# Kernel optimization log

Hardware: AMD Instinct MI355X
Metric: run time of the kernel (lower is better)

Reference implementation:

```python
import jax, jax.numpy as jnp
import numpy as np

EPS = 1e-5


def _conv1x1_3d(x, w, b):
    # x: [B,C,T,H,W], w: [O,C], b: [O]  (Conv3d with kernel 1)
    return jnp.einsum('bcthw,oc->bothw', x, w) + b[None, :, None, None, None]


def _nonlocal_layer(x, Kw, Kb, Qw, Qb, Vw, Vb, Ow, Ob, gamma, beta, in_dim):
    K = _conv1x1_3d(x, Kw, Kb)
    Q = _conv1x1_3d(x, Qw, Qb)
    V = _conv1x1_3d(x, Vw, Vb)
    B, C, T, H, W = K.shape
    S = T * H * W
    Kf = K.reshape(B, C, S)
    Qf = Q.reshape(B, C, S)
    Vf = V.reshape(B, C, S)
    # KQ[b,s,t] = sum_c K[b,c,s] Q[b,c,t];  attn = softmax over t
    attn = jax.nn.softmax(jnp.einsum('bcs,bct->bst', Kf, Qf) / np.sqrt(in_dim).astype(np.float32), axis=2)
    # original broadcast pattern: (V.view(B,C,S,1) * attn[:,None]).sum(3)
    #   == V[b,c,s] * sum_t attn[b,s,t]  (rows of softmax sum to ~1)
    Vn = Vf * attn.sum(axis=2)[:, None, :]
    Vn = jax.nn.relu(Vn).reshape(B, C, T, H, W)
    O = jax.nn.relu(_conv1x1_3d(Vn, Ow, Ob))
    y = x + O
    # BatchNorm3d in training mode: per-channel batch statistics
    mu = y.mean(axis=(0, 2, 3, 4), keepdims=True)
    var = y.var(axis=(0, 2, 3, 4), keepdims=True)
    return gamma[None, :, None, None, None] * (y - mu) / jnp.sqrt(var + EPS) + beta[None, :, None, None, None]


def _conv_transpose_2x2_s2(x, w, b):
    # torch ConvTranspose2d(k=2, stride=2): weight [Cin, Cout, 2, 2]; output pixels don't overlap
    N, C, H, W = x.shape
    O = w.shape[1]
    y = jnp.einsum('nchw,codk->nohdwk', x, w).reshape(N, O, 2 * H, 2 * W)
    return y + b[None, :, None, None]


def _positional_encoding(S, D):
    position = jnp.arange(S, dtype=jnp.float32)[:, None]
    div_term = jnp.exp(jnp.arange(0, D, 2, dtype=jnp.float32) * (-np.log(10000.0) / D))
    pe = jnp.zeros((S, D), dtype=jnp.float32)
    pe = pe.at[:, 0::2].set(jnp.sin(position * div_term))
    pe = pe.at[:, 1::2].set(jnp.cos(position * div_term))
    return pe  # [S, D]


def setup_inputs() -> dict:
    key = jax.random.key(0)
    ks = jax.random.split(key, 24)
    B, Tc, Hc, Wc = 8, 6, 12, 12
    Tf, Hf, Wf = 4, 12, 12
    Din, Dff, Dout, L = 1024, 512, 128, 2
    s = 0.02
    inp = {
        'context': jax.random.normal(ks[0], (B, Tc, Din, Hc, Wc), jnp.float32),
        'frame': jax.random.normal(ks[1], (B, Tf, Din, Hf, Wf), jnp.float32),
        'nl_Kw': jax.random.normal(ks[2], (L, Dff, Din), jnp.float32) * s,
        'nl_Kb': jnp.zeros((L, Dff), jnp.float32),
        'nl_Qw': jax.random.normal(ks[3], (L, Dff, Din), jnp.float32) * s,
        'nl_Qb': jnp.zeros((L, Dff), jnp.float32),
        'nl_Vw': jax.random.normal(ks[4], (L, Dff, Din), jnp.float32) * s,
        'nl_Vb': jnp.zeros((L, Dff), jnp.float32),
        'nl_Ow': jax.random.normal(ks[5], (L, Din, Dff), jnp.float32) * s,
        'nl_Ob': jnp.zeros((L, Din), jnp.float32),
        'nl_gamma': jnp.ones((L, Din), jnp.float32),
        'nl_beta': jnp.zeros((L, Din), jnp.float32),
        'tp_w': jax.random.normal(ks[6], (Dout, Din, 3, 3, 3), jnp.float32) * s,
        'tp_b': jnp.zeros((Dout,), jnp.float32),
        'up1_w': jax.random.normal(ks[7], (Din, Dff, 2, 2), jnp.float32) * s,
        'up1_b': jnp.zeros((Dff,), jnp.float32),
        'up2_w': jax.random.normal(ks[8], (Dff, Dout, 2, 2), jnp.float32) * s,
        'up2_b': jnp.zeros((Dout,), jnp.float32),
    }
    return inp


def reference(context, frame, nl_Kw, nl_Kb, nl_Qw, nl_Qb, nl_Vw, nl_Vb, nl_Ow, nl_Ob,
              nl_gamma, nl_beta, tp_w, tp_b, up1_w, up1_b, up2_w, up2_b):
    in_dim = context.shape[2]
    out_dim = up2_w.shape[1]
    # ---- non-local layers over context ----
    x = jnp.swapaxes(context, 1, 2)  # [B, C, T, H, W]
    n_layers = nl_Kw.shape[0]
    for l in range(n_layers):
        x = _nonlocal_layer(x, nl_Kw[l], nl_Kb[l], nl_Qw[l], nl_Qb[l], nl_Vw[l], nl_Vb[l],
                            nl_Ow[l], nl_Ob[l], nl_gamma[l], nl_beta[l], in_dim)
    # ---- temporal pool (Conv3d k=3, VALID) + ReLU + global avg pool ----
    g = jax.lax.conv_general_dilated(x, tp_w, (1, 1, 1), 'VALID',
                                     dimension_numbers=('NCDHW', 'OIDHW', 'NCDHW'))
    g = jax.nn.relu(g + tp_b[None, :, None, None, None])
    goal_embed = g.mean(axis=(2, 3, 4))  # [B, out_dim]
    # ---- upsample frame ----
    B, Tf, C, H, W = frame.shape
    fr = frame.reshape(B * Tf, C, H, W)
    h = jax.nn.relu(_conv_transpose_2x2_s2(fr, up1_w, up1_b))
    h = _conv_transpose_2x2_s2(h, up2_w, up2_b)  # [B*Tf, out_dim, 4H, 4W]
    N = B * Tf
    S = H * W * 16
    state_embed = h.reshape(N, out_dim, S)
    # ---- positional encoding on V ----
    pe = _positional_encoding(S, out_dim)  # [S, D]
    V = jnp.transpose(state_embed, (0, 2, 1)) + pe[None, :, :]  # [N, S, D]
    # ---- goal/state attention (note: torch .repeat tiles t-major, kept faithful) ----
    goal_rep = jnp.tile(goal_embed, (Tf, 1))  # [Tf*B, D], index t*B+b
    SG = jnp.einsum('nds,nd->ns', state_embed, goal_rep) / np.sqrt(out_dim).astype(np.float32)
    attn = jax.nn.softmax(SG, axis=1)  # [N, S]
    state_goal_attn = jnp.einsum('ns,nsd->nd', attn, V).reshape(B, Tf, out_dim)
    return (goal_embed, state_goal_attn)
```

## Files before the change

kernel.cpp:

```cpp
#include <hip/hip_runtime.h>
#include <cstddef>
#include <cstdint>


static constexpr int B_ = 8, TC = 6, TF = 4, DIN = 1024, DFF = 512, DOUT = 128;
static constexpr int HWP = 144;
static constexpr int P_CTX = B_ * TC * HWP;
static constexpr int NF = B_ * TF;
static constexpr int P_FRM = NF * HWP;
static constexpr int P_H1 = NF * 24 * 24;
static constexpr int P_H2 = NF * 48 * 48;
static constexpr int S2 = 48 * 48;
static constexpr int NPOS = 3200;

static constexpr size_t OFF_XB   = 0;
static constexpr size_t OFF_YB   = 3538944;
static constexpr size_t OFF_VNB  = 7077888;
static constexpr size_t OFF_WB1  = 8847360;
static constexpr size_t OFF_WB2  = 9371648;
static constexpr size_t OFF_TWB  = 9900032;
static constexpr size_t OFF_W1B  = 11669504;
static constexpr size_t OFF_W2B  = 12718080;
static constexpr size_t OFF_ST   = 12849152;
static constexpr size_t OFF_GP   = 12849152;
static constexpr size_t OFF_R    = 18378752;
static constexpr size_t OFF_HP1B = 18788352;
static constexpr size_t OFF_F0B  = 23506944;
static constexpr size_t OFF_HP2B = 0;
static constexpr size_t OFF_SG   = 14692352;
static constexpr size_t OFF_PE   = 7077888;

typedef __attribute__((ext_vector_type(8))) short bf16x8;
typedef __attribute__((ext_vector_type(4))) float f32x4;
typedef __attribute__((ext_vector_type(4))) unsigned short us4;
typedef __attribute__((ext_vector_type(8))) unsigned short us8;

__device__ __forceinline__ unsigned short f2b(float f) {
    union { float f; uint32_t u; } x{f};
    uint32_t r = x.u + 0x7FFFu + ((x.u >> 16) & 1u);
    return (unsigned short)(r >> 16);
}
__device__ __forceinline__ float b2f(unsigned short u) {
    union { uint32_t u; float f; } x;
    x.u = (uint32_t)u << 16;
    return x.f;
}

#define GL16(g, s)                                                        \
    __builtin_amdgcn_global_load_lds(                                     \
        (const __attribute__((address_space(1))) void*)(g),               \
        (__attribute__((address_space(3))) void*)(s), 16, 0, 0)

static constexpr int PW0 = 4 * 524288;
static constexpr int PW1 = PW0 + 27 * 1024 * 128;
static constexpr int PW2 = PW1 + 4 * 512 * 1024;
static constexpr int PW3 = PW2 + 4 * 128 * 512;
static constexpr int NB_PREP = PW3 / 256;
static constexpr int NB_CTXT = 9 * 16 * (B_ * TC);
static constexpr int NB_FRMT = 9 * 16 * NF;
static constexpr int NB_STZ  = 32;

__device__ __forceinline__ void transpose_body(const float* __restrict__ in,
                                               unsigned short* __restrict__ outB,
                                               int C, int HW, int bx, int by, int bz,
                                               float (*T)[17]) {
    int tid = threadIdx.x;
    int tx = tid & 15, ty = tid >> 4;
    int f = bz, hw0 = bx * 16, c0 = by * 64;
#pragma unroll
    for (int i = 0; i < 4; ++i)
        T[ty + 16 * i][tx] = in[((size_t)f * C + c0 + ty + 16 * i) * HW + hw0 + tx];
    __syncthreads();
#pragma unroll
    for (int i = 0; i < 4; ++i)
        outB[((size_t)f * HW + hw0 + ty) * C + c0 + tx + 16 * i] = f2b(T[tx + 16 * i][ty]);
}

__global__ __launch_bounds__(256) void prep_all(
    const float* __restrict__ Vw, const float* __restrict__ Ow,
    const float* __restrict__ tp, const float* __restrict__ u1w,
    const float* __restrict__ u2w,
    const float* __restrict__ context, const float* __restrict__ frame,
    unsigned short* __restrict__ WB1, unsigned short* __restrict__ WB2,
    unsigned short* __restrict__ TWB, unsigned short* __restrict__ W1B,
    unsigned short* __restrict__ W2B,
    unsigned short* __restrict__ XB, unsigned short* __restrict__ F0B,
    float* __restrict__ ST) {
    __shared__ float T[64][17];
    int b = blockIdx.x;
    if (b < NB_PREP) {
        int t = b * 256 + threadIdx.x;
        if (t < PW0) {
            int which = t >> 19;
            int r = t & 524287;
            int kr = r & 7;
            int layer = which >> 1;
            if ((which & 1) == 0) {
                int o = (r >> 3) & 511, kg = (r >> 3) >> 9;
                WB1[(size_t)layer * 524288 + r] =
                    f2b(Vw[(size_t)layer * 524288 + (size_t)o * 1024 + kg * 8 + kr]);
            } else {
                int o = (r >> 3) & 1023, kg = (r >> 3) >> 10;
                WB2[(size_t)layer * 524288 + r] =
                    f2b(Ow[(size_t)layer * 524288 + (size_t)o * 512 + kg * 8 + kr]);
            }
        } else if (t < PW1) {
            int r = t - PW0;
            int kr = r & 7, o = (r >> 3) & 127, kg = (r >> 10) & 127, tap = r >> 17;
            int c = kg * 8 + kr;
            TWB[r] = f2b(tp[((size_t)o * 1024 + c) * 27 + tap]);
        } else if (t < PW2) {
            int r = t - PW1;
            int kr = r & 7, o = (r >> 3) % 512;
            int rest = (r >> 3) / 512;
            int kg = rest & 127, d = rest >> 7;
            W1B[r] = f2b(u1w[((size_t)(kg * 8 + kr) * 512 + o) * 4 + d]);
        } else if (t < PW3) {
            int r = t - PW2;
            int kr = r & 7, o = (r >> 3) & 127;
            int rest = (r >> 3) >> 7;
            int kg = rest & 63, d = rest >> 6;
            W2B[r] = f2b(u2w[((size_t)(kg * 8 + kr) * 128 + o) * 4 + d]);
        }
    } else if (b < NB_PREP + NB_CTXT) {
        int bb = b - NB_PREP;
        transpose_body(context, XB, DIN, HWP, bb % 9, (bb / 9) % 16, bb / 144, T);
    } else if (b < NB_PREP + NB_CTXT + NB_FRMT) {
        int bb = b - NB_PREP - NB_CTXT;
        transpose_body(frame, F0B, DIN, HWP, bb % 9, (bb / 9) % 16, bb / 144, T);
    } else {
        int idx = (b - NB_PREP - NB_CTXT - NB_FRMT) * 256 + threadIdx.x;
        ST[idx] = 0.f;
    }
}

template <int EPI, int REMAP, int GATHER, int MT>
__device__ __forceinline__ void gemm_body(
    const unsigned short* __restrict__ A, const unsigned short* __restrict__ Bp,
    const float* __restrict__ bias, const unsigned short* __restrict__ resid,
    void* __restrict__ Cv, float* __restrict__ stats, int M, int N, int K,
    size_t bStrideZ, size_t cStrideZ,
    int inW, int inHW, int outW, int outSPP,
    int bx, int by, int bz,
    unsigned short* AlP, unsigned short* BlP, int* sPix) {
    constexpr int MI = MT / 32;
    constexpr int AL = MT / 64;
    constexpr int ASZ = MT * 32;
    int tid = threadIdx.x;
    int w = tid >> 6, l = tid & 63;
    int m0 = by * MT, n0 = bx * 128;
    int z = bz;
    const unsigned short* Bpz = Bp + (size_t)z * bStrideZ;

    if (GATHER) {
        if (tid < MT) {
            int pos = m0 + tid;
            int ww = pos % 10;
            int r = pos / 10;
            int h = r % 10;
            r /= 10;
            int t = r & 3, b = r >> 2;
            int dt = z / 9, rr = z - dt * 9;
            int doff = dt * 144 + (rr / 3) * 12 + (rr % 3);
            sPix[tid] = ((b * 6 + t) * 12 + h) * 12 + ww + doff;
        }
        __syncthreads();
    }

    int wr = w >> 1, wc = w & 1;
    int l15 = l & 15, lg = l >> 4;

    float bv[4];
#pragma unroll
    for (int ni = 0; ni < 4; ++ni)
        bv[ni] = (EPI & 1) ? bias[n0 + wc * 64 + ni * 16 + l15] : 0.f;
    asm volatile("s_waitcnt vmcnt(0)" ::: "memory");

    const unsigned short* ag[AL];
    int aoff[AL];
#pragma unroll
    for (int a = 0; a < AL; ++a) {
        int row = l + a * 64;
        int grow = GATHER ? sPix[row] : (m0 + row);
        ag[a] = A + (size_t)grow * K + w * 8;
        aoff[a] = (w * MT + row) * 8;
    }
    int bkg = tid >> 7, bn = tid & 127;
    const unsigned short* bg0 = Bpz + ((size_t)bkg * N + n0 + bn) * 8;
    const unsigned short* bg1 = Bpz + ((size_t)(bkg + 2) * N + n0 + bn) * 8;
    const int boff0 = tid * 8, boff1 = (tid + 256) * 8;
    size_t bstep = (size_t)32 * N;

    f32x4 acc[MI][4];
#pragma unroll
    for (int mi = 0; mi < MI; ++mi)
#pragma unroll
        for (int ni = 0; ni < 4; ++ni) acc[mi][ni] = (f32x4){0.f, 0.f, 0.f, 0.f};

    int nt = K >> 5;
#pragma unroll
    for (int a = 0; a < AL; ++a) { GL16(ag[a], &AlP[aoff[a]]); ag[a] += 32; }
    GL16(bg0, &BlP[boff0]);
    GL16(bg1, &BlP[boff1]);
    bg0 += bstep; bg1 += bstep;
#pragma unroll
    for (int a = 0; a < AL; ++a) { GL16(ag[a], &AlP[ASZ + aoff[a]]); ag[a] += 32; }
    GL16(bg0, &BlP[4096 + boff0]);
    GL16(bg1, &BlP[4096 + boff1]);
    bg0 += bstep; bg1 += bstep;

    int bc = 0, sb = 2;
    for (int t = 0; t < nt; ++t) {
        __builtin_amdgcn_s_barrier();
        if (t + 2 < nt) {
#pragma unroll
            for (int a = 0; a < AL; ++a) { GL16(ag[a], &AlP[sb * ASZ + aoff[a]]); ag[a] += 32; }
            GL16(bg0, &BlP[sb * 4096 + boff0]);
            GL16(bg1, &BlP[sb * 4096 + boff1]);
            bg0 += bstep; bg1 += bstep;
            if (MT == 128)
                asm volatile("s_waitcnt vmcnt(8)" ::: "memory");
            else
                asm volatile("s_waitcnt vmcnt(6)" ::: "memory");
        } else if (t + 2 == nt) {
            if (MT == 128)
                asm volatile("s_waitcnt vmcnt(4)" ::: "memory");
            else
                asm volatile("s_waitcnt vmcnt(3)" ::: "memory");
        } else {
            asm volatile("s_waitcnt vmcnt(0)" ::: "memory");
        }
        __builtin_amdgcn_sched_barrier(0);
        bf16x8 af[MI], bf[4];
#pragma unroll
        for (int mi = 0; mi < MI; ++mi)
            af[mi] = *(const bf16x8*)&AlP[bc * ASZ + (lg * MT + wr * (MT / 2) + mi * 16 + l15) * 8];
#pragma unroll
        for (int ni = 0; ni < 4; ++ni)
            bf[ni] = *(const bf16x8*)&BlP[bc * 4096 + (lg * 128 + wc * 64 + ni * 16 + l15) * 8];
        __builtin_amdgcn_s_setprio(1);
#pragma unroll
        for (int mi = 0; mi < MI; ++mi)
#pragma unroll
            for (int ni = 0; ni < 4; ++ni)
                acc[mi][ni] = __builtin_amdgcn_mfma_f32_16x16x32_bf16(
                    af[mi], bf[ni], acc[mi][ni], 0, 0, 0);
        __builtin_amdgcn_s_setprio(0);
        __builtin_amdgcn_sched_barrier(0);
        bc = (bc == 2) ? 0 : bc + 1;
        sb = (sb == 2) ? 0 : sb + 1;
    }

    float* Cf = (float*)Cv + (size_t)z * cStrideZ;
    unsigned short* Cb = (unsigned short*)Cv + (size_t)z * cStrideZ;
    float sacc[4] = {0, 0, 0, 0}, qacc[4] = {0, 0, 0, 0};
#pragma unroll
    for (int mi = 0; mi < MI; ++mi) {
#pragma unroll
        for (int r = 0; r < 4; ++r) {
            int m = m0 + wr * (MT / 2) + mi * 16 + lg * 4 + r;
            int orow = m;
            if (REMAP) {
                int ni_ = m / inHW;
                int rem = m - ni_ * inHW;
                int h = rem / inW, ww = rem - h * inW;
                orow = ni_ * outSPP + (2 * h + (z >> 1)) * outW + (2 * ww + (z & 1));
            }
#pragma unroll
            for (int ni = 0; ni < 4; ++ni) {
                int n = n0 + wc * 64 + ni * 16 + l15;
                float v = acc[mi][ni][r] + bv[ni];
                if (EPI & 2) v = fmaxf(v, 0.f);
                if (EPI & 4) v += b2f(resid[(size_t)m * N + n]);
                if (EPI & 16) { sacc[ni] += v; qacc[ni] += v * v; }
                if (EPI & 8)
                    Cb[(size_t)orow * N + n] = f2b(v);
                else
                    Cf[(size_t)orow * N + n] = v;
            }
        }
    }
    if (EPI & 16) {
        __syncthreads();
        float* sred = (float*)AlP;
        sred[tid] = 0.f;
        __syncthreads();
#pragma unroll
        for (int ni = 0; ni < 4; ++ni) {
            int c = wc * 64 + ni * 16 + l15;
            atomicAdd(&sred[c], sacc[ni]);
            atomicAdd(&sred[128 + c], qacc[ni]);
        }
        __syncthreads();
        if (tid < 128)
            atomicAdd(&stats[n0 + tid], sred[tid]);
        else
            atomicAdd(&stats[1024 + n0 + (tid & 127)], sred[tid]);
    }
}

template <int EPI, int REMAP, int GATHER, int MT>
__global__ __launch_bounds__(256) void gemm_mfma(
    const unsigned short* __restrict__ A, const unsigned short* __restrict__ Bp,
    const float* __restrict__ bias, const unsigned short* __restrict__ resid,
    void* __restrict__ Cv, float* __restrict__ stats, int M, int N, int K,
    size_t bStrideZ, size_t cStrideZ,
    int inW, int inHW, int outW, int outSPP) {
    __shared__ unsigned short Al[3 * MT * 32];
    __shared__ unsigned short Bl[3 * 128 * 32];
    __shared__ int sPix[MT];
    gemm_body<EPI, REMAP, GATHER, MT>(A, Bp, bias, resid, Cv, stats, M, N, K,
                                      bStrideZ, cStrideZ, inW, inHW, outW, outSPP,
                                      blockIdx.x, blockIdx.y, blockIdx.z,
                                      Al, Bl, sPix);
}

__global__ __launch_bounds__(256) void conv3_up1(
    const unsigned short* __restrict__ XB, const unsigned short* __restrict__ TWB,
    unsigned short* __restrict__ GP,
    const unsigned short* __restrict__ F0B, const unsigned short* __restrict__ W1B,
    const float* __restrict__ u1b, unsigned short* __restrict__ HP1B) {
    __shared__ unsigned short Al[3 * 128 * 32];
    __shared__ unsigned short Bl[3 * 128 * 32];
    __shared__ int sPix[128];
    if (blockIdx.x < 680) {
        int xcd = blockIdx.x & 7, k = blockIdx.x >> 3;
        int wcnt = (xcd < 3) ? 85 : 84;
        if (k >= wcnt) return;
        int wk = (xcd < 3) ? xcd * 85 + k : 255 + (xcd - 3) * 84 + k;
        gemm_body<8, 0, 1, 128>(XB, TWB, nullptr, nullptr, GP, nullptr,
                                NPOS, DOUT, DIN,
                                (size_t)DIN / 8 * DOUT * 8, (size_t)NPOS * DOUT,
                                0, 0, 0, 0, 0, wk / 27, wk % 27, Al, Bl, sPix);
    } else {
        int b = blockIdx.x - 680;
        gemm_body<11, 1, 0, 128>(F0B, W1B, u1b, nullptr, HP1B, nullptr,
                                 P_FRM, DFF, DIN,
                                 (size_t)DIN / 8 * DFF * 8, 0, 12, 144, 24, 576,
                                 b & 3, (b >> 2) % 36, b / 144, Al, Bl, sPix);
    }
}

__global__ __launch_bounds__(256) void up2_tail(
    const unsigned short* __restrict__ HP1B, const unsigned short* __restrict__ W2B,
    const float* __restrict__ u2b, unsigned short* __restrict__ HP2B,
    const unsigned short* __restrict__ Gp, const float* __restrict__ tpb,
    float* __restrict__ R, float* __restrict__ PE, float* __restrict__ out) {
    __shared__ unsigned short Al[3 * 128 * 32];
    __shared__ unsigned short Bl[3 * 128 * 32];
    __shared__ int sPix[128];
    int b = blockIdx.x;
    if (b < 576) {
        gemm_body<9, 1, 0, 128>(HP1B, W2B, u2b, nullptr, HP2B, nullptr,
                                P_H1, DOUT, DFF,
                                (size_t)DFF / 8 * DOUT * 8, 0, 24, 576, 48, 2304,
                                0, b % 144, b / 144, Al, Bl, sPix);
    } else if (b < 2176) {
        int idx = (b - 576) * 256 + threadIdx.x;
        float s = 0.f;
        for (int tap = 0; tap < 27; ++tap) s += b2f(Gp[(size_t)tap * (NPOS * 128) + idx]);
        R[idx] = fmaxf(s + tpb[idx & 127], 0.f);
    } else if (b < 3328) {
        int idx = (b - 2176) * 256 + threadIdx.x;
        int s = idx >> 7, d = idx & 127;
        float freq = expf(-(float)(d & ~1) * (9.210340371976184f / 128.f));
        float ang = (float)s * freq;
        PE[idx] = (d & 1) ? cosf(ang) : sinf(ang);
    } else {
        int idx = (b - 3328) * 256 + threadIdx.x;
        out[1024 + idx] = 0.f;
    }
}

__global__ __launch_bounds__(128) void goal_reduce(const float* __restrict__ R,
                                                   float* __restrict__ out) {
    int b = blockIdx.x, o = threadIdx.x;
    float s = 0.f;
    for (int i = 0; i < 400; ++i) s += R[(size_t)(b * 400 + i) * 128 + o];
    out[b * 128 + o] = s * (1.f / 400.f);
}


__global__ __launch_bounds__(256) void bn_final(float* __restrict__ st,
                                                const float* __restrict__ gamma,
                                                const float* __restrict__ beta) {
    int c = blockIdx.x * 256 + threadIdx.x;
    if (c >= 1024) return;
    const float invn = 1.f / 6912.f;
    float mean = st[c] * invn;
    float var = st[1024 + c] * invn - mean * mean;
    float sc = gamma[c] * rsqrtf(var + 1e-5f);
    st[2048 + c] = sc;
    st[3072 + c] = beta[c] - mean * sc;
}

__global__ __launch_bounds__(256) void bn_apply_b(const unsigned short* __restrict__ YB,
                                                  unsigned short* __restrict__ XB,
                                                  const float* __restrict__ st) {
    const float* scale = st + 2048;
    const float* shift = st + 3072;
    int idx = blockIdx.x * 256 + threadIdx.x;
    int c0 = (idx & 255) << 2;
    us4 y = ((const us4*)YB)[idx];
    us4 o;
#pragma unroll
    for (int j = 0; j < 4; ++j) o[j] = f2b(b2f(y[j]) * scale[c0 + j] + shift[c0 + j]);
    ((us4*)XB)[idx] = o;
}


__global__ __launch_bounds__(256) void attn_logits(const unsigned short* __restrict__ Hp2,
                                                   const float* __restrict__ out,
                                                   float* __restrict__ SG) {
    int n = blockIdx.y;
    int tid = threadIdx.x;
    int s = blockIdx.x * 16 + (tid >> 4);
    int l16 = tid & 15;
    us8 row = *((const us8*)(Hp2 + ((size_t)n * S2 + s) * 128) + l16);
    const float* g = out + (n & 7) * 128 + l16 * 8;
    float dot = 0.f;
#pragma unroll
    for (int i = 0; i < 8; ++i) dot += b2f(row[i]) * g[i];
    dot += __shfl_xor(dot, 1);
    dot += __shfl_xor(dot, 2);
    dot += __shfl_xor(dot, 4);
    dot += __shfl_xor(dot, 8);
    if (l16 == 0) SG[(size_t)n * S2 + s] = dot * 0.0883883476483184f;
}

__global__ __launch_bounds__(256) void attn_softmax(float* __restrict__ SG) {
    __shared__ float red[256];
    int n = blockIdx.x, tid = threadIdx.x;
    float* row = SG + (size_t)n * S2;
    float v[9];
    float lmax = -3.4e38f;
#pragma unroll
    for (int i = 0; i < 9; ++i) {
        v[i] = row[tid + 256 * i];
        lmax = fmaxf(lmax, v[i]);
    }
    red[tid] = lmax;
    __syncthreads();
    for (int off = 128; off > 0; off >>= 1) {
        if (tid < off) red[tid] = fmaxf(red[tid], red[tid + off]);
        __syncthreads();
    }
    float m = red[0];
    __syncthreads();
    float ls = 0.f;
#pragma unroll
    for (int i = 0; i < 9; ++i) {
        v[i] = expf(v[i] - m);
        ls += v[i];
    }
    red[tid] = ls;
    __syncthreads();
    for (int off = 128; off > 0; off >>= 1) {
        if (tid < off) red[tid] += red[tid + off];
        __syncthreads();
    }
    float inv = 1.f / red[0];
#pragma unroll
    for (int i = 0; i < 9; ++i) row[tid + 256 * i] = v[i] * inv;
}

__global__ __launch_bounds__(256) void attn_pv(const unsigned short* __restrict__ Hp2,
                                               const float* __restrict__ SG,
                                               const float* __restrict__ PE,
                                               float* __restrict__ out) {
    int n = blockIdx.y;
    int sb = blockIdx.x;
    int tid = threadIdx.x;
    int d = tid & 127, half = tid >> 7;
    int s0 = sb * 128 + half * 64;
    const float* att = SG + (size_t)n * S2;
    float acc = 0.f;
    for (int i = 0; i < 64; ++i) {
        int s = s0 + i;
        acc += att[s] * (b2f(Hp2[((size_t)n * S2 + s) * 128 + d]) + PE[(size_t)s * 128 + d]);
    }
    atomicAdd(&out[1024 + n * 128 + d], acc);
}


extern "C" void kernel_launch(void* const* d_in, const int* in_sizes, int n_in,
                              void* d_out, int out_size, void* d_ws, size_t ws_size,
                              hipStream_t stream) {
    const float* context = (const float*)d_in[0];
    const float* frame = (const float*)d_in[1];
    const float* Vw = (const float*)d_in[6];
    const float* Vb = (const float*)d_in[7];
    const float* Ow = (const float*)d_in[8];
    const float* Ob = (const float*)d_in[9];
    const float* gamma = (const float*)d_in[10];
    const float* beta = (const float*)d_in[11];
    const float* tpw = (const float*)d_in[12];
    const float* tpb = (const float*)d_in[13];
    const float* u1w = (const float*)d_in[14];
    const float* u1b = (const float*)d_in[15];
    const float* u2w = (const float*)d_in[16];
    const float* u2b = (const float*)d_in[17];
    float* ws = (float*)d_ws;
    float* out = (float*)d_out;

    unsigned short* XB = (unsigned short*)(ws + OFF_XB);
    unsigned short* YB = (unsigned short*)(ws + OFF_YB);
    unsigned short* VNB = (unsigned short*)(ws + OFF_VNB);
    unsigned short* WB1 = (unsigned short*)(ws + OFF_WB1);
    unsigned short* WB2 = (unsigned short*)(ws + OFF_WB2);
    float* ST = ws + OFF_ST;
    unsigned short* TWB = (unsigned short*)(ws + OFF_TWB);
    unsigned short* W1B = (unsigned short*)(ws + OFF_W1B);
    unsigned short* W2B = (unsigned short*)(ws + OFF_W2B);
    unsigned short* GP = (unsigned short*)(ws + OFF_GP);
    float* R = ws + OFF_R;
    unsigned short* F0B = (unsigned short*)(ws + OFF_F0B);
    unsigned short* HP1B = (unsigned short*)(ws + OFF_HP1B);
    unsigned short* HP2B = (unsigned short*)(ws + OFF_HP2B);
    float* SG = ws + OFF_SG;
    float* PE = ws + OFF_PE;

    prep_all<<<NB_PREP + NB_CTXT + NB_FRMT + NB_STZ, 256, 0, stream>>>(
        Vw, Ow, tpw, u1w, u2w, context, frame, WB1, WB2, TWB, W1B, W2B,
        XB, F0B, ST);

    for (int l = 0; l < 2; ++l) {
        float* STl = ST + (size_t)l * 4096;
        gemm_mfma<11, 0, 0, 64><<<dim3(DFF / 128, P_CTX / 64, 1), 256, 0, stream>>>(
            XB, WB1 + (size_t)l * 524288, Vb + l * DFF, nullptr, VNB, nullptr,
            P_CTX, DFF, DIN, 0, 0, 0, 0, 0, 0);
        gemm_mfma<31, 0, 0, 128><<<dim3(DIN / 128, P_CTX / 128, 1), 256, 0, stream>>>(
            VNB, WB2 + (size_t)l * 524288, Ob + l * DIN, XB, YB, STl,
            P_CTX, DIN, DFF, 0, 0, 0, 0, 0, 0);
        bn_final<<<4, 256, 0, stream>>>(STl, gamma + l * DIN, beta + l * DIN);
        bn_apply_b<<<(P_CTX * DIN / 4) / 256, 256, 0, stream>>>(YB, XB, STl);
    }

    conv3_up1<<<680 + 576, 256, 0, stream>>>(XB, TWB, GP, F0B, W1B, u1b, HP1B);

    up2_tail<<<576 + 1600 + 1152 + 16, 256, 0, stream>>>(HP1B, W2B, u2b, HP2B,
                                                         GP, tpb, R, PE, out);
    goal_reduce<<<8, 128, 0, stream>>>(R, out);

    attn_logits<<<dim3(S2 / 16, NF), 256, 0, stream>>>(HP2B, out, SG);
    attn_softmax<<<NF, 256, 0, stream>>>(SG);
    attn_pv<<<dim3(18, NF), 256, 0, stream>>>(HP2B, SG, PE, out);
}
```

Before: 262.6 us.

## Fuse BN finalize into apply, fuse softmax into PV, remap up1 block order

Folds the per-channel BatchNorm scale/shift computation into the apply kernel, which removes one launch per layer but recomputes the stats for every element. Merges the softmax kernel into the attention PV kernel: each block recomputes the row max and sum itself, then applies exp on the fly, removing a launch and the write-back of normalized probabilities. Remaps the block index for the up1 GEMM so tiles are grouped across XCDs for better cache locality. The cost is redundant reductions and extra exp work per block.

```diff
diff --git a/kernel.cpp b/kernel.cpp
--- a/kernel.cpp
+++ b/kernel.cpp
@@ -333,11 +333,13 @@
                                 (size_t)DIN / 8 * DOUT * 8, (size_t)NPOS * DOUT,
                                 0, 0, 0, 0, 0, wk / 27, wk % 27, Al, Bl, sPix);
     } else {
-        int b = blockIdx.x - 680;
+        int lb = blockIdx.x - 680;
+        int wk = (lb & 7) * 72 + (lb >> 3);
+        int mt = wk >> 4, rest = wk & 15;
         gemm_body<11, 1, 0, 128>(F0B, W1B, u1b, nullptr, HP1B, nullptr,
                                  P_FRM, DFF, DIN,
                                  (size_t)DIN / 8 * DFF * 8, 0, 12, 144, 24, 576,
-                                 b & 3, (b >> 2) % 36, b / 144, Al, Bl, sPix);
+                                 rest & 3, mt, rest >> 2, Al, Bl, sPix);
     }
 }
 
@@ -380,31 +382,25 @@
     out[b * 128 + o] = s * (1.f / 400.f);
 }
 
-
-__global__ __launch_bounds__(256) void bn_final(float* __restrict__ st,
-                                                const float* __restrict__ gamma,
-                                                const float* __restrict__ beta) {
-    int c = blockIdx.x * 256 + threadIdx.x;
-    if (c >= 1024) return;
-    const float invn = 1.f / 6912.f;
-    float mean = st[c] * invn;
-    float var = st[1024 + c] * invn - mean * mean;
-    float sc = gamma[c] * rsqrtf(var + 1e-5f);
-    st[2048 + c] = sc;
-    st[3072 + c] = beta[c] - mean * sc;
-}
-
 __global__ __launch_bounds__(256) void bn_apply_b(const unsigned short* __restrict__ YB,
                                                   unsigned short* __restrict__ XB,
-                                                  const float* __restrict__ st) {
-    const float* scale = st + 2048;
-    const float* shift = st + 3072;
+                                                  const float* __restrict__ st,
+                                                  const float* __restrict__ gamma,
+                                                  const float* __restrict__ beta) {
     int idx = blockIdx.x * 256 + threadIdx.x;
     int c0 = (idx & 255) << 2;
+    const float invn = 1.f / 6912.f;
     us4 y = ((const us4*)YB)[idx];
     us4 o;
 #pragma unroll
-    for (int j = 0; j < 4; ++j) o[j] = f2b(b2f(y[j]) * scale[c0 + j] + shift[c0 + j]);
+    for (int j = 0; j < 4; ++j) {
+        int c = c0 + j;
+        float mean = st[c] * invn;
+        float var = st[1024 + c] * invn - mean * mean;
+        float sc = gamma[c] * rsqrtf(var + 1e-5f);
+        float sh = beta[c] - mean * sc;
+        o[j] = f2b(b2f(y[j]) * sc + sh);
+    }
     ((us4*)XB)[idx] = o;
 }
 
@@ -428,17 +424,18 @@
     if (l16 == 0) SG[(size_t)n * S2 + s] = dot * 0.0883883476483184f;
 }
 
-__global__ __launch_bounds__(256) void attn_softmax(float* __restrict__ SG) {
+__global__ __launch_bounds__(256) void attn_pv(const unsigned short* __restrict__ Hp2,
+                                               const float* __restrict__ SG,
+                                               const float* __restrict__ PE,
+                                               float* __restrict__ out) {
     __shared__ float red[256];
-    int n = blockIdx.x, tid = threadIdx.x;
-    float* row = SG + (size_t)n * S2;
-    float v[9];
+    int n = blockIdx.y;
+    int sb = blockIdx.x;
+    int tid = threadIdx.x;
+    const float* att = SG + (size_t)n * S2;
     float lmax = -3.4e38f;
 #pragma unroll
-    for (int i = 0; i < 9; ++i) {
-        v[i] = row[tid + 256 * i];
-        lmax = fmaxf(lmax, v[i]);
-    }
+    for (int i = 0; i < 9; ++i) lmax = fmaxf(lmax, att[tid + 256 * i]);
     red[tid] = lmax;
     __syncthreads();
     for (int off = 128; off > 0; off >>= 1) {
@@ -449,10 +446,7 @@
     __syncthreads();
     float ls = 0.f;
 #pragma unroll
-    for (int i = 0; i < 9; ++i) {
-        v[i] = expf(v[i] - m);
-        ls += v[i];
-    }
+    for (int i = 0; i < 9; ++i) ls += expf(att[tid + 256 * i] - m);
     red[tid] = ls;
     __syncthreads();
     for (int off = 128; off > 0; off >>= 1) {
@@ -460,24 +454,13 @@
         __syncthreads();
     }
     float inv = 1.f / red[0];
-#pragma unroll
-    for (int i = 0; i < 9; ++i) row[tid + 256 * i] = v[i] * inv;
-}
-
-__global__ __launch_bounds__(256) void attn_pv(const unsigned short* __restrict__ Hp2,
-                                               const float* __restrict__ SG,
-                                               const float* __restrict__ PE,
-                                               float* __restrict__ out) {
-    int n = blockIdx.y;
-    int sb = blockIdx.x;
-    int tid = threadIdx.x;
     int d = tid & 127, half = tid >> 7;
     int s0 = sb * 128 + half * 64;
-    const float* att = SG + (size_t)n * S2;
     float acc = 0.f;
     for (int i = 0; i < 64; ++i) {
         int s = s0 + i;
-        acc += att[s] * (b2f(Hp2[((size_t)n * S2 + s) * 128 + d]) + PE[(size_t)s * 128 + d]);
+        float p = expf(att[s] - m) * inv;
+        acc += p * (b2f(Hp2[((size_t)n * S2 + s) * 128 + d]) + PE[(size_t)s * 128 + d]);
     }
     atomicAdd(&out[1024 + n * 128 + d], acc);
 }
@@ -532,8 +515,8 @@
         gemm_mfma<31, 0, 0, 128><<<dim3(DIN / 128, P_CTX / 128, 1), 256, 0, stream>>>(
             VNB, WB2 + (size_t)l * 524288, Ob + l * DIN, XB, YB, STl,
             P_CTX, DIN, DFF, 0, 0, 0, 0, 0, 0);
-        bn_final<<<4, 256, 0, stream>>>(STl, gamma + l * DIN, beta + l * DIN);
-        bn_apply_b<<<(P_CTX * DIN / 4) / 256, 256, 0, stream>>>(YB, XB, STl);
+        bn_apply_b<<<(P_CTX * DIN / 4) / 256, 256, 0, stream>>>(
+            YB, XB, STl, gamma + l * DIN, beta + l * DIN);
     }
 
     conv3_up1<<<680 + 576, 256, 0, stream>>>(XB, TWB, GP, F0B, W1B, u1b, HP1B);
@@ -543,6 +526,5 @@
     goal_reduce<<<8, 128, 0, stream>>>(R, out);
 
     attn_logits<<<dim3(S2 / 16, NF), 256, 0, stream>>>(HP2B, out, SG);
-    attn_softmax<<<NF, 256, 0, stream>>>(SG);
     attn_pv<<<dim3(18, NF), 256, 0, stream>>>(HP2B, SG, PE, out);
 }
```

Result: no change. 263.1 us (+0.2%).
